# Optimization experiments

Measured on AMD Instinct MI355X. Metric: run time of the kernel, lower is better.

## Reference

```python
import jax, jax.numpy as jnp
import numpy as np

B, Q, S, D, H = 8, 100, 4096, 256, 8
HD = D // H
EPS = 1e-5


def layer_norm(x, g, b):
    mu = jnp.mean(x, axis=-1, keepdims=True)
    var = jnp.mean(jnp.square(x - mu), axis=-1, keepdims=True)
    return (x - mu) * jax.lax.rsqrt(var + EPS) * g + b


def mha(q_in, k_in, v_in, w_in, b_in, w_out, b_out, bias=None):
    # torch nn.MultiheadAttention math (batch_first, dropout=0)
    wq, wk, wv = jnp.split(w_in, 3, axis=0)
    bq, bk, bv = jnp.split(b_in, 3, axis=0)
    Bq, Lq, _ = q_in.shape
    Lk = k_in.shape[1]
    q = (q_in @ wq.T + bq).reshape(Bq, Lq, H, HD)
    k = (k_in @ wk.T + bk).reshape(Bq, Lk, H, HD)
    v = (v_in @ wv.T + bv).reshape(Bq, Lk, H, HD)
    scores = jnp.einsum('bqhd,bkhd->bhqk', q, k) / jnp.sqrt(jnp.asarray(HD, q.dtype))
    if bias is not None:
        scores = scores + bias  # [B,1,Q,S] broadcast over heads (same per head)
    attn = jax.nn.softmax(scores, axis=-1)
    out = jnp.einsum('bhqk,bkhd->bqhd', attn, v).reshape(Bq, Lq, D)
    return out @ w_out.T + b_out


def setup_inputs() -> dict:
    key = jax.random.key(0)
    ks = jax.random.split(key, 12)
    s = 0.02
    return {
        'queries': jax.random.normal(ks[0], (B, Q, D), jnp.float32),
        'pixel_feat': jax.random.normal(ks[1], (B, S, D), jnp.float32),
        'prev_mask': jax.random.normal(ks[2], (B, Q, S), jnp.float32),
        'cross_in_w': jax.random.normal(ks[3], (3 * D, D), jnp.float32) * s,
        'cross_in_b': jnp.zeros((3 * D,), jnp.float32),
        'cross_out_w': jax.random.normal(ks[4], (D, D), jnp.float32) * s,
        'cross_out_b': jnp.zeros((D,), jnp.float32),
        'self_in_w': jax.random.normal(ks[5], (3 * D, D), jnp.float32) * s,
        'self_in_b': jnp.zeros((3 * D,), jnp.float32),
        'self_out_w': jax.random.normal(ks[6], (D, D), jnp.float32) * s,
        'self_out_b': jnp.zeros((D,), jnp.float32),
        'ln_cross_g': jnp.ones((D,), jnp.float32),
        'ln_cross_b': jnp.zeros((D,), jnp.float32),
        'ln_self_g': jnp.ones((D,), jnp.float32),
        'ln_self_b': jnp.zeros((D,), jnp.float32),
        'ln_ffn_g': jnp.ones((D,), jnp.float32),
        'ln_ffn_b': jnp.zeros((D,), jnp.float32),
        'ffn_w1': jax.random.normal(ks[7], (4 * D, D), jnp.float32) * s,
        'ffn_b1': jnp.zeros((4 * D,), jnp.float32),
        'ffn_w2': jax.random.normal(ks[8], (D, 4 * D), jnp.float32) * s,
        'ffn_b2': jnp.zeros((D,), jnp.float32),
    }


def reference(queries, pixel_feat, prev_mask,
              cross_in_w, cross_in_b, cross_out_w, cross_out_b,
              self_in_w, self_in_b, self_out_w, self_out_b,
              ln_cross_g, ln_cross_b, ln_self_g, ln_self_b, ln_ffn_g, ln_ffn_b,
              ffn_w1, ffn_b1, ffn_w2, ffn_b2):
    # masked cross-attn bias (no-grad region in torch; boolean ops have no grad)
    region = jax.nn.sigmoid(prev_mask) > 0.5                    # [B,Q,S]
    any_pos = jnp.any(region, axis=-1, keepdims=True)
    region = jnp.where(any_pos, region, jnp.ones_like(region))
    bias = (~region).astype(queries.dtype) * -10000.0
    bias = bias[:, None, :, :]                                  # [B,1,Q,S]

    q_out = mha(layer_norm(queries, ln_cross_g, ln_cross_b), pixel_feat, pixel_feat,
                cross_in_w, cross_in_b, cross_out_w, cross_out_b, bias)
    queries = queries + q_out

    q_norm = layer_norm(queries, ln_self_g, ln_self_b)
    q_out = mha(q_norm, q_norm, q_norm, self_in_w, self_in_b, self_out_w, self_out_b)
    queries = queries + q_out

    h = layer_norm(queries, ln_ffn_g, ln_ffn_b)
    h = jax.nn.gelu(h @ ffn_w1.T + ffn_b1, approximate=False) @ ffn_w2.T + ffn_b2
    return queries + h
```

## Files before the change

### kernel.cpp

```cpp
#include <hip/hip_runtime.h>
#include <hip/hip_bf16.h>
#include <math.h>

#define BQ 100
#define SB 8
#define SS 4096
#define DD 256
#define HH 8
#define HDD 32
#define NSPLIT 4
#define SCHUNK (SS / NSPLIT)
#define MROWS 800

typedef __attribute__((ext_vector_type(8))) short bf16x8;
typedef __attribute__((ext_vector_type(4))) float f32x4;

__device__ inline unsigned short f2bf(float f) {
    union { float f; unsigned u; } v; v.f = f;
    unsigned r = v.u + 0x7fff + ((v.u >> 16) & 1);
    return (unsigned short)(r >> 16);
}

__device__ inline unsigned pkbf(float x, float y) {
    union { __hip_bfloat162 h; unsigned u; } c;
    c.h = __float22bfloat162_rn(make_float2(x, y));
    return c.u;
}

__device__ inline bf16x8 load_bf8(const float* p) {
    float4 a = *(const float4*)p;
    float4 b = *(const float4*)(p + 4);
    union { unsigned u[4]; bf16x8 v; } r;
    r.u[0] = pkbf(a.x, a.y); r.u[1] = pkbf(a.z, a.w);
    r.u[2] = pkbf(b.x, b.y); r.u[3] = pkbf(b.z, b.w);
    return r.v;
}

typedef __attribute__((address_space(1))) const void gas_void;
typedef __attribute__((address_space(3))) void las_void;
__device__ inline void gl_lds16(const unsigned short* g, unsigned short* l) {
    __builtin_amdgcn_global_load_lds((gas_void*)g, (las_void*)l, 16, 0, 0);
}

#define TM 128
#define TN 128

#define WOFF_CW   0
#define WOFF_SIW  196608
#define WOFF_COW  393216
#define WOFF_SOW  458752
#define WOFF_F1   524288
#define WOFF_F2   786432
#define WTOT      1048576

__global__ __launch_bounds__(256) void wprep(
        const float* __restrict__ cw, const float* __restrict__ siw,
        const float* __restrict__ cow, const float* __restrict__ sow,
        const float* __restrict__ f1, const float* __restrict__ f2,
        const float* __restrict__ pix,
        unsigned short* __restrict__ o, unsigned short* __restrict__ abf) {
    int b = blockIdx.x;
    int t = threadIdx.x;
    if (b >= 512) {
        size_t off = (size_t)(b - 512) * 2048 + (size_t)t * 8;
        const float* p = pix + off;
        float4 a = *(const float4*)p;
        float4 c = *(const float4*)(p + 4);
        uint4 pk;
        pk.x = pkbf(a.x, a.y); pk.y = pkbf(a.z, a.w);
        pk.z = pkbf(c.x, c.y); pk.w = pkbf(c.z, c.w);
        *(uint4*)(abf + off) = pk;
        return;
    }
    const float* src; size_t so, doff;
    if (b < 96)       { src = cw;  so = (size_t)b * 2048;         doff = WOFF_CW; }
    else if (b < 192) { src = siw; so = (size_t)(b - 96) * 2048;  doff = WOFF_SIW; }
    else if (b < 224) { src = cow; so = (size_t)(b - 192) * 2048; doff = WOFF_COW; }
    else if (b < 256) { src = sow; so = (size_t)(b - 224) * 2048; doff = WOFF_SOW; }
    else if (b < 384) { src = f1;  so = (size_t)(b - 256) * 2048; doff = WOFF_F1; }
    else              { src = f2;  so = (size_t)(b - 384) * 2048; doff = WOFF_F2; }
    const float* p = src + so + (size_t)t * 8;
    float4 a = *(const float4*)p;
    float4 c = *(const float4*)(p + 4);
    uint4 pk;
    pk.x = pkbf(a.x, a.y); pk.y = pkbf(a.z, a.w);
    pk.z = pkbf(c.x, c.y); pk.w = pkbf(c.z, c.w);
    *(uint4*)(o + doff + so + (size_t)t * 8) = pk;
}

__global__ __launch_bounds__(256, 3) void stage1(
        const float* __restrict__ queries,
        const float* __restrict__ ln_g, const float* __restrict__ ln_b,
        const unsigned short* __restrict__ wbf,
        const float* __restrict__ cb,
        float* __restrict__ q_cross,
        const unsigned short* __restrict__ Abf,
        unsigned short* __restrict__ Kb, unsigned short* __restrict__ Vb,
        const float* __restrict__ mask, unsigned* __restrict__ Mbits) {
    __shared__ __align__(16) char smem[32768];
    const int bid = blockIdx.x;
    const int t = threadIdx.x;

    if (bid < 1024) {
        unsigned short* Sbuf = (unsigned short*)smem;
        const unsigned short* Wb = wbf + (size_t)DD * DD;
        const float* bias = cb + DD;
        int xcd = bid & 7, idx = bid >> 3;
        int mtile = xcd + 8 * (idx >> 2);
        int ntl = idx & 3;
        int m0 = mtile * TM, n0 = ntl * TN;
        int wave = t >> 6, lane = t & 63;
        int wm = (wave & 1) * 64, wn = (wave >> 1) * 64;
        int fr = lane & 15, quad = lane >> 4;
        f32x4 acc[4][4] = {};

        const int c0 = t, c1 = 256 + t;
        const int r0 = c0 >> 2, r1 = c1 >> 2;
        const int cc0 = (c0 & 3) ^ ((r0 >> 1) & 3);
        const int cc1 = (c1 & 3) ^ ((r1 >> 1) & 3);

        gl_lds16(Abf + (size_t)(m0 + r0) * DD + cc0 * 8, Sbuf + c0 * 8);
        gl_lds16(Abf + (size_t)(m0 + r1) * DD + cc1 * 8, Sbuf + c1 * 8);
        gl_lds16(Wb + (size_t)(n0 + r0) * DD + cc0 * 8, Sbuf + 4096 + c0 * 8);
        gl_lds16(Wb + (size_t)(n0 + r1) * DD + cc1 * 8, Sbuf + 4096 + c1 * 8);
        __syncthreads();

#pragma unroll
        for (int ks = 0; ks < 8; ks++) {
            unsigned short* Ab = Sbuf + (ks & 1) * 8192;
            unsigned short* Bb = Ab + 4096;
            if (ks < 7) {
                unsigned short* An = Sbuf + ((ks + 1) & 1) * 8192;
                unsigned short* Bn = An + 4096;
                int k0 = (ks + 1) * 32;
                gl_lds16(Abf + (size_t)(m0 + r0) * DD + k0 + cc0 * 8, An + c0 * 8);
                gl_lds16(Abf + (size_t)(m0 + r1) * DD + k0 + cc1 * 8, An + c1 * 8);
                gl_lds16(Wb + (size_t)(n0 + r0) * DD + k0 + cc0 * 8, Bn + c0 * 8);
                gl_lds16(Wb + (size_t)(n0 + r1) * DD + k0 + cc1 * 8, Bn + c1 * 8);
            }
            bf16x8 af[4], bv[4];
#pragma unroll
            for (int mi = 0; mi < 4; mi++) {
                int row = wm + mi * 16 + fr;
                int j = quad ^ ((row >> 1) & 3);
                af[mi] = *(const bf16x8*)(Ab + row * 32 + j * 8);
            }
#pragma unroll
            for (int ni = 0; ni < 4; ni++) {
                int row = wn + ni * 16 + fr;
                int j = quad ^ ((row >> 1) & 3);
                bv[ni] = *(const bf16x8*)(Bb + row * 32 + j * 8);
            }
#pragma unroll
            for (int mi = 0; mi < 4; mi++) {
                acc[mi][0] = __builtin_amdgcn_mfma_f32_16x16x32_bf16(af[mi], bv[0], acc[mi][0], 0, 0, 0);
                acc[mi][1] = __builtin_amdgcn_mfma_f32_16x16x32_bf16(af[mi], bv[1], acc[mi][1], 0, 0, 0);
                acc[mi][2] = __builtin_amdgcn_mfma_f32_16x16x32_bf16(af[mi], bv[2], acc[mi][2], 0, 0, 0);
                acc[mi][3] = __builtin_amdgcn_mfma_f32_16x16x32_bf16(af[mi], bv[3], acc[mi][3], 0, 0, 0);
            }
            __syncthreads();
        }
#pragma unroll
        for (int ni = 0; ni < 4; ni++) {
            int n = n0 + wn + ni * 16 + fr;
            float bv = bias[n];
            unsigned short* dst = (n < 256) ? Kb : Vb;
            int hh = (n >> 5) & 7, d = n & 31;
#pragma unroll
            for (int mi = 0; mi < 4; mi++) {
#pragma unroll
                for (int r = 0; r < 4; r++) {
                    int m = m0 + wm + mi * 16 + quad * 4 + r;
                    int bb = m >> 12, s = m & (SS - 1);
                    dst[((((size_t)bb * HH + hh) * SS + s) << 5) + d] =
                        f2bf(acc[mi][ni][r] + bv);
                }
            }
        }
    } else if (bid < 1824) {
        int row = bid - 1024;
        unsigned* words = (unsigned*)smem;
        unsigned* orred = (unsigned*)(smem + 512);
        int w = t >> 6, lane = t & 63;
        const float* mp = mask + (size_t)row * SS + lane;
        float mv[16];
#pragma unroll
        for (int i = 0; i < 16; i++) mv[i] = mp[(w * 16 + i) * 64];
        unsigned lor = 0;
#pragma unroll
        for (int i = 0; i < 16; i++) {
            unsigned long long bal = __ballot(mv[i] > 0.f);
            if (lane == 0) {
                words[(w * 16 + i) * 2] = (unsigned)bal;
                words[(w * 16 + i) * 2 + 1] = (unsigned)(bal >> 32);
            }
            lor |= (unsigned)(bal | (bal >> 32));
        }
        if (lane == 0) orred[w] = lor;
        __syncthreads();
        unsigned anyv = orred[0] | orred[1] | orred[2] | orred[3];
        if (t < 128) Mbits[(size_t)row * 128 + t] = anyv ? words[t] : 0xFFFFFFFFu;
    } else {
        typedef unsigned short (*arow_t)[264];
        arow_t Aq = (arow_t)smem;
        float* mu_s = (float*)(smem + 16896);
        float* rs_s = mu_s + 32;
        float (*prt)[8][2] = (float(*)[8][2])(rs_s + 32);
        int idx = bid - 1824;
        int nq = idx & 1, my = idx >> 1;
        int m0 = my * 32;
        int row = t & 31, cs = t >> 5;
        const float* xp = queries + (size_t)(m0 + row) * DD + cs * 32;
        float s = 0.f, ss = 0.f;
#pragma unroll
        for (int c = 0; c < 32; c += 4) {
            float4 v = *(const float4*)(xp + c);
            s += v.x + v.y + v.z + v.w;
            ss += v.x * v.x + v.y * v.y + v.z * v.z + v.w * v.w;
        }
        prt[row][cs][0] = s; prt[row][cs][1] = ss;
        __syncthreads();
        if (t < 32) {
            float sum = 0.f, sq = 0.f;
#pragma unroll
            for (int k = 0; k < 8; k++) { sum += prt[t][k][0]; sq += prt[t][k][1]; }
            float mu = sum * (1.0f / DD);
            float var = sq * (1.0f / DD) - mu * mu;
            mu_s[t] = mu;
            rs_s[t] = rsqrtf(var + 1e-5f);
        }
        __syncthreads();
        {
            float mu = mu_s[row], r = rs_s[row];
            int col0 = cs * 32;
#pragma unroll
            for (int c = 0; c < 32; c += 8) {
                int col = col0 + c;
                float4 v0 = *(const float4*)(xp + c);
                float4 v1 = *(const float4*)(xp + c + 4);
                float4 g0 = *(const float4*)(ln_g + col);
                float4 g1 = *(const float4*)(ln_g + col + 4);
                float4 b0 = *(const float4*)(ln_b + col);
                float4 b1 = *(const float4*)(ln_b + col + 4);
                uint4 pk;
                pk.x = pkbf((v0.x - mu) * r * g0.x + b0.x, (v0.y - mu) * r * g0.y + b0.y);
                pk.y = pkbf((v0.z - mu) * r * g0.z + b0.z, (v0.w - mu) * r * g0.w + b0.w);
                pk.z = pkbf((v1.x - mu) * r * g1.x + b1.x, (v1.y - mu) * r * g1.y + b1.y);
                pk.w = pkbf((v1.z - mu) * r * g1.z + b1.z, (v1.w - mu) * r * g1.w + b1.w);
                *(uint4*)&Aq[row][col] = pk;
            }
        }
        __syncthreads();
        int w = t >> 6, lane = t & 63;
        int fr = lane & 15, quad = lane >> 4;
        int n0 = nq * 128 + w * 32;
        f32x4 acc[2][2] = {};
        const unsigned short* Wq0 = wbf + (size_t)(n0 + fr) * DD + quad * 8;
        const unsigned short* Wq1 = Wq0 + (size_t)16 * DD;
#pragma unroll
        for (int k0 = 0; k0 < DD; k0 += 32) {
            bf16x8 a0 = *(const bf16x8*)&Aq[fr][k0 + quad * 8];
            bf16x8 a1 = *(const bf16x8*)&Aq[16 + fr][k0 + quad * 8];
            bf16x8 w0 = *(const bf16x8*)(Wq0 + k0);
            bf16x8 w1 = *(const bf16x8*)(Wq1 + k0);
            acc[0][0] = __builtin_amdgcn_mfma_f32_16x16x32_bf16(a0, w0, acc[0][0], 0, 0, 0);
            acc[0][1] = __builtin_amdgcn_mfma_f32_16x16x32_bf16(a0, w1, acc[0][1], 0, 0, 0);
            acc[1][0] = __builtin_amdgcn_mfma_f32_16x16x32_bf16(a1, w0, acc[1][0], 0, 0, 0);
            acc[1][1] = __builtin_amdgcn_mfma_f32_16x16x32_bf16(a1, w1, acc[1][1], 0, 0, 0);
        }
#pragma unroll
        for (int ni = 0; ni < 2; ni++) {
            int n = n0 + ni * 16 + fr;
            float bv = cb[n];
#pragma unroll
            for (int mi = 0; mi < 2; mi++) {
#pragma unroll
                for (int r = 0; r < 4; r++) {
                    int m = m0 + mi * 16 + quad * 4 + r;
                    q_cross[(size_t)m * DD + n] = acc[mi][ni][r] + bv;
                }
            }
        }
    }
}

template<int MODE>
__global__ __launch_bounds__(64, 4) void ln_gemm(
        const float* __restrict__ X, const float* __restrict__ gam,
        const float* __restrict__ bet,
        const unsigned short* __restrict__ W, const float* __restrict__ bias,
        const float* __restrict__ res,
        float* __restrict__ C, int N) {
    __shared__ unsigned short As[32][264];
    __shared__ float mu_s[32], rs_s[32];
    __shared__ float prt[32][2][2];
    const int t = threadIdx.x;
    const int fr = t & 15, quad = t >> 4;
    const int m0 = blockIdx.y * 32, n0 = blockIdx.x * 32;
    const int row = t & 31, half = t >> 5;

    const float* xp = X + (size_t)(m0 + row) * DD + half * 128;
    float s = 0.f, ss = 0.f;
#pragma unroll
    for (int c = 0; c < 128; c += 4) {
        float4 v = *(const float4*)(xp + c);
        s += v.x + v.y + v.z + v.w;
        ss += v.x * v.x + v.y * v.y + v.z * v.z + v.w * v.w;
    }
    prt[row][half][0] = s;
    prt[row][half][1] = ss;
    __syncthreads();
    if (t < 32) {
        float sum = prt[t][0][0] + prt[t][1][0];
        float sq  = prt[t][0][1] + prt[t][1][1];
        float mu = sum * (1.0f / DD);
        float var = sq * (1.0f / DD) - mu * mu;
        mu_s[t] = mu;
        rs_s[t] = rsqrtf(var + 1e-5f);
    }
    __syncthreads();
    {
        float mu = mu_s[row], r = rs_s[row];
#pragma unroll
        for (int c = 0; c < 128; c += 8) {
            int col = half * 128 + c;
            float4 v0 = *(const float4*)(xp + c);
            float4 v1 = *(const float4*)(xp + c + 4);
            float4 g0 = *(const float4*)(gam + col);
            float4 g1 = *(const float4*)(gam + col + 4);
            float4 b0 = *(const float4*)(bet + col);
            float4 b1 = *(const float4*)(bet + col + 4);
            uint4 pk;
            pk.x = pkbf((v0.x - mu) * r * g0.x + b0.x, (v0.y - mu) * r * g0.y + b0.y);
            pk.y = pkbf((v0.z - mu) * r * g0.z + b0.z, (v0.w - mu) * r * g0.w + b0.w);
            pk.z = pkbf((v1.x - mu) * r * g1.x + b1.x, (v1.y - mu) * r * g1.y + b1.y);
            pk.w = pkbf((v1.z - mu) * r * g1.z + b1.z, (v1.w - mu) * r * g1.w + b1.w);
            *(uint4*)&As[row][col] = pk;
        }
    }
    __syncthreads();

    f32x4 acc[2][2] = {};
    const unsigned short* Wp0 = W + (size_t)(n0 + fr) * DD + quad * 8;
    const unsigned short* Wp1 = Wp0 + (size_t)16 * DD;
#pragma unroll
    for (int k0 = 0; k0 < DD; k0 += 32) {
        bf16x8 a0 = *(const bf16x8*)&As[fr][k0 + quad * 8];
        bf16x8 a1 = *(const bf16x8*)&As[16 + fr][k0 + quad * 8];
        bf16x8 w0 = *(const bf16x8*)(Wp0 + k0);
        bf16x8 w1 = *(const bf16x8*)(Wp1 + k0);
        acc[0][0] = __builtin_amdgcn_mfma_f32_16x16x32_bf16(a0, w0, acc[0][0], 0, 0, 0);
        acc[0][1] = __builtin_amdgcn_mfma_f32_16x16x32_bf16(a0, w1, acc[0][1], 0, 0, 0);
        acc[1][0] = __builtin_amdgcn_mfma_f32_16x16x32_bf16(a1, w0, acc[1][0], 0, 0, 0);
        acc[1][1] = __builtin_amdgcn_mfma_f32_16x16x32_bf16(a1, w1, acc[1][1], 0, 0, 0);
    }

#pragma unroll
    for (int ni = 0; ni < 2; ni++) {
        int n = n0 + ni * 16 + fr;
        float bv = bias[n];
#pragma unroll
        for (int mi = 0; mi < 2; mi++) {
#pragma unroll
            for (int r = 0; r < 4; r++) {
                int m = m0 + mi * 16 + quad * 4 + r;
                float v = acc[mi][ni][r] + bv;
                if (MODE == 1) {
                    v = 0.5f * v * (1.0f + erff(v * 0.70710678118654752f));
                } else if (MODE == 2) {
                    v += res[(size_t)m * N + n];
                }
                C[(size_t)m * N + n] = v;
            }
        }
    }
}

__global__ __launch_bounds__(64, 4) void comb_gemm(
        const float* __restrict__ Opart, const float* __restrict__ mpart,
        const float* __restrict__ lpart,
        const unsigned short* __restrict__ W, const float* __restrict__ bias,
        const float* __restrict__ res,
        float* __restrict__ C) {
    __shared__ unsigned short As[32][264];
    const int t = threadIdx.x;
    const int fr = t & 15, quad = t >> 4;
    const int m0 = blockIdx.y * 32, n0 = blockIdx.x * 32;
    const int row = t & 31, half = t >> 5;

    {
        int m = m0 + row;
        int b = m / BQ, q = m % BQ;
#pragma unroll
        for (int h = half * 4; h < half * 4 + 4; h++) {
            float mv[NSPLIT], wsp[NSPLIT];
            float mstar = -1e30f;
#pragma unroll
            for (int sp = 0; sp < NSPLIT; sp++) {
                mv[sp] = mpart[((size_t)(b * NSPLIT + sp) * HH + h) * BQ + q];
                mstar = fmaxf(mstar, mv[sp]);
            }
            float lstar = 0.f;
#pragma unroll
            for (int sp = 0; sp < NSPLIT; sp++) {
                wsp[sp] = __expf(mv[sp] - mstar);
                lstar += lpart[((size_t)(b * NSPLIT + sp) * HH + h) * BQ + q] * wsp[sp];
            }
            float inv = 1.0f / lstar;
#pragma unroll
            for (int d = 0; d < HDD; d += 8) {
                float o[8] = {};
#pragma unroll
                for (int sp = 0; sp < NSPLIT; sp++) {
                    const float* op = Opart +
                        ((size_t)(b * NSPLIT + sp) * BQ + q) * DD + h * HDD + d;
                    float4 a = *(const float4*)op;
                    float4 b4 = *(const float4*)(op + 4);
                    o[0] += a.x * wsp[sp];  o[1] += a.y * wsp[sp];
                    o[2] += a.z * wsp[sp];  o[3] += a.w * wsp[sp];
                    o[4] += b4.x * wsp[sp]; o[5] += b4.y * wsp[sp];
                    o[6] += b4.z * wsp[sp]; o[7] += b4.w * wsp[sp];
                }
                uint4 pk;
                pk.x = pkbf(o[0] * inv, o[1] * inv);
                pk.y = pkbf(o[2] * inv, o[3] * inv);
                pk.z = pkbf(o[4] * inv, o[5] * inv);
                pk.w = pkbf(o[6] * inv, o[7] * inv);
                *(uint4*)&As[row][h * HDD + d] = pk;
            }
        }
    }
    __syncthreads();

    f32x4 acc[2][2] = {};
    const unsigned short* Wp0 = W + (size_t)(n0 + fr) * DD + quad * 8;
    const unsigned short* Wp1 = Wp0 + (size_t)16 * DD;
#pragma unroll
    for (int k0 = 0; k0 < DD; k0 += 32) {
        bf16x8 a0 = *(const bf16x8*)&As[fr][k0 + quad * 8];
        bf16x8 a1 = *(const bf16x8*)&As[16 + fr][k0 + quad * 8];
        bf16x8 w0 = *(const bf16x8*)(Wp0 + k0);
        bf16x8 w1 = *(const bf16x8*)(Wp1 + k0);
        acc[0][0] = __builtin_amdgcn_mfma_f32_16x16x32_bf16(a0, w0, acc[0][0], 0, 0, 0);
        acc[0][1] = __builtin_amdgcn_mfma_f32_16x16x32_bf16(a0, w1, acc[0][1], 0, 0, 0);
        acc[1][0] = __builtin_amdgcn_mfma_f32_16x16x32_bf16(a1, w0, acc[1][0], 0, 0, 0);
        acc[1][1] = __builtin_amdgcn_mfma_f32_16x16x32_bf16(a1, w1, acc[1][1], 0, 0, 0);
    }

#pragma unroll
    for (int ni = 0; ni < 2; ni++) {
        int n = n0 + ni * 16 + fr;
        float bv = bias[n];
#pragma unroll
        for (int mi = 0; mi < 2; mi++) {
#pragma unroll
            for (int r = 0; r < 4; r++) {
                int m = m0 + mi * 16 + quad * 4 + r;
                float v = acc[mi][ni][r] + bv + res[(size_t)m * DD + n];
                C[(size_t)m * DD + n] = v;
            }
        }
    }
}

template<int KK, int SPLITK, int MODE>
__global__ __launch_bounds__(64, 4) void gemm_skinny2(
        const float* __restrict__ A, const unsigned short* __restrict__ W,
        const float* __restrict__ bias, const float* __restrict__ res,
        float* __restrict__ C, float* __restrict__ Cp, int N) {
    const int lane = threadIdx.x;
    const int fr = lane & 15, quad = lane >> 4;
    const int m0 = blockIdx.y * 32;
    const int n0 = blockIdx.x * 32;
    const int sk = blockIdx.z;
    const int KCH = KK / SPLITK;

    f32x4 acc[2][2] = {};
    const float* Ap0 = A + (size_t)(m0 + fr) * KK + sk * KCH + quad * 8;
    const float* Ap1 = Ap0 + (size_t)16 * KK;
    const unsigned short* Wp0 = W + (size_t)(n0 + fr) * KK + sk * KCH + quad * 8;
    const unsigned short* Wp1 = Wp0 + (size_t)16 * KK;

#pragma unroll
    for (int k0 = 0; k0 < KCH; k0 += 32) {
        bf16x8 a0 = load_bf8(Ap0 + k0);
        bf16x8 a1 = load_bf8(Ap1 + k0);
        bf16x8 w0 = *(const bf16x8*)(Wp0 + k0);
        bf16x8 w1 = *(const bf16x8*)(Wp1 + k0);
        acc[0][0] = __builtin_amdgcn_mfma_f32_16x16x32_bf16(a0, w0, acc[0][0], 0, 0, 0);
        acc[0][1] = __builtin_amdgcn_mfma_f32_16x16x32_bf16(a0, w1, acc[0][1], 0, 0, 0);
        acc[1][0] = __builtin_amdgcn_mfma_f32_16x16x32_bf16(a1, w0, acc[1][0], 0, 0, 0);
        acc[1][1] = __builtin_amdgcn_mfma_f32_16x16x32_bf16(a1, w1, acc[1][1], 0, 0, 0);
    }

    if (SPLITK == 1) {
#pragma unroll
        for (int ni = 0; ni < 2; ni++) {
            int n = n0 + ni * 16 + fr;
            float bv = bias[n];
#pragma unroll
            for (int mi = 0; mi < 2; mi++) {
#pragma unroll
                for (int r = 0; r < 4; r++) {
                    int m = m0 + mi * 16 + quad * 4 + r;
                    float v = acc[mi][ni][r] + bv;
                    if (MODE == 1) {
                        v = 0.5f * v * (1.0f + erff(v * 0.70710678118654752f));
                    } else if (MODE == 2) {
                        v += res[(size_t)m * N + n];
                    }
                    C[(size_t)m * N + n] = v;
                }
            }
        }
    } else {
        float* dst = Cp + (size_t)sk * MROWS * N;
#pragma unroll
        for (int ni = 0; ni < 2; ni++) {
            int n = n0 + ni * 16 + fr;
#pragma unroll
            for (int mi = 0; mi < 2; mi++) {
#pragma unroll
                for (int r = 0; r < 4; r++) {
                    int m = m0 + mi * 16 + quad * 4 + r;
                    dst[(size_t)m * N + n] = acc[mi][ni][r];
                }
            }
        }
    }
}

template<int SPLITK, int MODE>
__global__ void gemm_combine(const float* __restrict__ Cp,
                             const float* __restrict__ bias,
                             const float* __restrict__ res,
                             float* __restrict__ C, int N) {
    int m = blockIdx.x;
    for (int n = threadIdx.x; n < N; n += 256) {
        float v = bias[n];
#pragma unroll
        for (int sk = 0; sk < SPLITK; sk++)
            v += Cp[((size_t)sk * MROWS + m) * N + n];
        if (MODE == 1) {
            v = 0.5f * v * (1.0f + erff(v * 0.70710678118654752f));
        } else if (MODE == 2) {
            v += res[(size_t)m * N + n];
        }
        C[(size_t)m * N + n] = v;
    }
}

#define QT 64
#define ST 128

__global__ __launch_bounds__(256) void cross_attn_mfma(
        const float* __restrict__ Qm,
        const unsigned short* __restrict__ Kb,
        const unsigned short* __restrict__ Vb,
        const unsigned* __restrict__ Mbits,
        float* __restrict__ Opart,
        float* __restrict__ mpart,
        float* __restrict__ lpart) {
    __shared__ unsigned short Qs[QT][40];
    __shared__ unsigned short Ks[ST][40];
    __shared__ unsigned short Vt[HDD][136];
    __shared__ unsigned short Ps[QT][136];
    __shared__ unsigned Mq[QT][4];
    __shared__ float red[QT][17];
    __shared__ float m_s[QT], alpha_s[QT], l_s[QT];

    const int qb = blockIdx.x, h = blockIdx.y;
    const int b = blockIdx.z / NSPLIT, sp = blockIdx.z % NSPLIT;
    const int t = threadIdx.x;
    const int w = t >> 6, lane = t & 63;
    const int fr = lane & 15, quad = lane >> 4;
    const int q0 = qb * QT;
    const int qlim = min(BQ - q0, QT);

    {
        int q = t >> 2, c0 = (t & 3) * 8;
        float4 v0 = make_float4(0.f, 0.f, 0.f, 0.f), v1 = v0;
        if (q < qlim) {
            const float* qp = Qm + (size_t)(b * BQ + q0 + q) * DD + h * HDD + c0;
            v0 = *(const float4*)qp;
            v1 = *(const float4*)(qp + 4);
        }
        const float sc = 0.17677669529663687f;
        uint4 pq;
        pq.x = pkbf(v0.x * sc, v0.y * sc);
        pq.y = pkbf(v0.z * sc, v0.w * sc);
        pq.z = pkbf(v1.x * sc, v1.y * sc);
        pq.w = pkbf(v1.z * sc, v1.w * sc);
        *(uint4*)&Qs[q][c0] = pq;
        if (t < QT) { m_s[t] = -1e30f; l_s[t] = 0.f; }
    }

    f32x4 oacc[2] = {};
    const unsigned short* Kbase = Kb + (((size_t)(b * HH + h)) * SS << 5);
    const unsigned short* Vbase = Vb + (((size_t)(b * HH + h)) * SS << 5);

    for (int s0 = sp * SCHUNK; s0 < (sp + 1) * SCHUNK; s0 += ST) {
        __syncthreads();
        {
            int r = t >> 1, half = t & 1;
            const unsigned short* kp = Kbase + ((size_t)(s0 + r) << 5) + half * 16;
            *(uint4*)&Ks[r][half * 16] = *(const uint4*)kp;
            *(uint4*)&Ks[r][half * 16 + 8] = *(const uint4*)(kp + 8);
            const unsigned short* vp = Vbase + ((size_t)(s0 + r) << 5) + half * 16;
            union { uint4 u; unsigned short s[8]; } v0, v1;
            v0.u = *(const uint4*)vp;
            v1.u = *(const uint4*)(vp + 8);
#pragma unroll
            for (int j = 0; j < 8; j++) Vt[half * 16 + j][r] = v0.s[j];
#pragma unroll
            for (int j = 0; j < 8; j++) Vt[half * 16 + 8 + j][r] = v1.s[j];
        }
        {
            int q = t >> 2, wd = t & 3;
            unsigned mword = 0xFFFFFFFFu;
            if (q < qlim)
                mword = Mbits[(size_t)(b * BQ + q0 + q) * 128 + (s0 >> 5) + wd];
            Mq[q][wd] = mword;
        }
        __syncthreads();

        bf16x8 af[2];
#pragma unroll
        for (int mt = 0; mt < 2; mt++)
            af[mt] = *(const bf16x8*)&Ks[w * 32 + mt * 16 + fr][quad * 8];
        f32x4 st[2][4];
#pragma unroll
        for (int nt = 0; nt < 4; nt++) {
            bf16x8 bq = *(const bf16x8*)&Qs[nt * 16 + fr][quad * 8];
#pragma unroll
            for (int mt = 0; mt < 2; mt++) {
                f32x4 z = {0.f, 0.f, 0.f, 0.f};
                st[mt][nt] = __builtin_amdgcn_mfma_f32_16x16x32_bf16(af[mt], bq, z, 0, 0, 0);
            }
        }

        float pmax[4] = {-1e30f, -1e30f, -1e30f, -1e30f};
#pragma unroll
        for (int nt = 0; nt < 4; nt++) {
            unsigned mword = Mq[nt * 16 + fr][w];
#pragma unroll
            for (int mt = 0; mt < 2; mt++)
#pragma unroll
                for (int r = 0; r < 4; r++) {
                    int bitpos = mt * 16 + quad * 4 + r;
                    float v = st[mt][nt][r];
                    if (!((mword >> bitpos) & 1u)) v -= 10000.f;
                    st[mt][nt][r] = v;
                    pmax[nt] = fmaxf(pmax[nt], v);
                }
        }
#pragma unroll
        for (int nt = 0; nt < 4; nt++)
            red[nt * 16 + fr][w * 4 + quad] = pmax[nt];
        __syncthreads();

        if (t < QT) {
            float mt_ = -1e30f;
#pragma unroll
            for (int k = 0; k < 16; k++) mt_ = fmaxf(mt_, red[t][k]);
            float mo = m_s[t], mn = fmaxf(mo, mt_);
            m_s[t] = mn;
            alpha_s[t] = __expf(mo - mn);
        }
        __syncthreads();

        float psum[4] = {0.f, 0.f, 0.f, 0.f};
#pragma unroll
        for (int nt = 0; nt < 4; nt++) {
            float mrow = m_s[nt * 16 + fr];
#pragma unroll
            for (int mt = 0; mt < 2; mt++) {
                float p0 = __expf(st[mt][nt][0] - mrow);
                float p1 = __expf(st[mt][nt][1] - mrow);
                float p2 = __expf(st[mt][nt][2] - mrow);
                float p3 = __expf(st[mt][nt][3] - mrow);
                psum[nt] += p0 + p1 + p2 + p3;
                uint2 pk;
                pk.x = pkbf(p0, p1);
                pk.y = pkbf(p2, p3);
                *(uint2*)&Ps[nt * 16 + fr][w * 32 + mt * 16 + quad * 4] = pk;
            }
        }
#pragma unroll
        for (int nt = 0; nt < 4; nt++)
            red[nt * 16 + fr][w * 4 + quad] = psum[nt];
        __syncthreads();

        if (t < QT) {
            float s = 0.f;
#pragma unroll
            for (int k = 0; k < 16; k++) s += red[t][k];
            l_s[t] = l_s[t] * alpha_s[t] + s;
        }

#pragma unroll
        for (int r = 0; r < 4; r++) {
            float a = alpha_s[w * 16 + quad * 4 + r];
            oacc[0][r] *= a; oacc[1][r] *= a;
        }
#pragma unroll
        for (int k0 = 0; k0 < ST; k0 += 32) {
            bf16x8 ap = *(const bf16x8*)&Ps[w * 16 + fr][k0 + quad * 8];
            bf16x8 bv0 = *(const bf16x8*)&Vt[fr][k0 + quad * 8];
            bf16x8 bv1 = *(const bf16x8*)&Vt[16 + fr][k0 + quad * 8];
            oacc[0] = __builtin_amdgcn_mfma_f32_16x16x32_bf16(ap, bv0, oacc[0], 0, 0, 0);
            oacc[1] = __builtin_amdgcn_mfma_f32_16x16x32_bf16(ap, bv1, oacc[1], 0, 0, 0);
        }
    }
    __syncthreads();

    int part = b * NSPLIT + sp;
    if (t < qlim) {
        mpart[((size_t)part * HH + h) * BQ + q0 + t] = m_s[t];
        lpart[((size_t)part * HH + h) * BQ + q0 + t] = l_s[t];
    }
#pragma unroll
    for (int nd = 0; nd < 2; nd++) {
#pragma unroll
        for (int r = 0; r < 4; r++) {
            int q = w * 16 + quad * 4 + r;
            if (q < qlim)
                Opart[((size_t)part * BQ + q0 + q) * DD + h * HDD + nd * 16 + fr] = oacc[nd][r];
        }
    }
}

__global__ __launch_bounds__(256) void self_attn_mfma(
        const float* __restrict__ qkv, float* __restrict__ Out) {
    __shared__ unsigned short Qs[128][40];
    __shared__ unsigned short Vt[HDD][136];
    __shared__ unsigned short Ps[112][136];
    __shared__ float red[112][17];
    __shared__ float m_s[112], l_s[112];

    const int h = blockIdx.x, b = blockIdx.y;
    const int t = threadIdx.x;
    const int w = t >> 6, lane = t & 63;
    const int fr = lane & 15, quad = lane >> 4;
    const float sc = 0.17677669529663687f;

    {
        int r = t >> 1, half = t & 1;
        float4 a0 = make_float4(0.f, 0.f, 0.f, 0.f), a1 = a0, a2 = a0, a3 = a0;
        float4 c0 = a0, c1 = a0, c2 = a0, c3 = a0;
        if (r < BQ) {
            const float* qp = qkv + (size_t)(b * BQ + r) * 768 + h * HDD + half * 16;
            a0 = *(const float4*)qp;       a1 = *(const float4*)(qp + 4);
            a2 = *(const float4*)(qp + 8); a3 = *(const float4*)(qp + 12);
            const float* vp = qp + 512;
            c0 = *(const float4*)vp;       c1 = *(const float4*)(vp + 4);
            c2 = *(const float4*)(vp + 8); c3 = *(const float4*)(vp + 12);
        }
        uint4 p0, p1;
        p0.x = pkbf(a0.x * sc, a0.y * sc); p0.y = pkbf(a0.z * sc, a0.w * sc);
        p0.z = pkbf(a1.x * sc, a1.y * sc); p0.w = pkbf(a1.z * sc, a1.w * sc);
        p1.x = pkbf(a2.x * sc, a2.y * sc); p1.y = pkbf(a2.z * sc, a2.w * sc);
        p1.z = pkbf(a3.x * sc, a3.y * sc); p1.w = pkbf(a3.z * sc, a3.w * sc);
        *(uint4*)&Qs[r][half * 16] = p0;
        *(uint4*)&Qs[r][half * 16 + 8] = p1;
        float vv[16] = {c0.x, c0.y, c0.z, c0.w, c1.x, c1.y, c1.z, c1.w,
                        c2.x, c2.y, c2.z, c2.w, c3.x, c3.y, c3.z, c3.w};
#pragma unroll
        for (int j = 0; j < 16; j++) Vt[half * 16 + j][r] = f2bf(vv[j]);
    }
    __syncthreads();

    bf16x8 af[2];
#pragma unroll
    for (int mt = 0; mt < 2; mt++) {
        int s = w * 32 + mt * 16 + fr;
        bf16x8 kz = {0, 0, 0, 0, 0, 0, 0, 0};
        af[mt] = kz;
        if (s < BQ)
            af[mt] = load_bf8(qkv + (size_t)(b * BQ + s) * 768 + 256 + h * HDD + quad * 8);
    }
    f32x4 st[2][7];
#pragma unroll
    for (int nt = 0; nt < 7; nt++) {
        bf16x8 bq = *(const bf16x8*)&Qs[nt * 16 + fr][quad * 8];
#pragma unroll
        for (int mt = 0; mt < 2; mt++) {
            f32x4 z = {0.f, 0.f, 0.f, 0.f};
            st[mt][nt] = __builtin_amdgcn_mfma_f32_16x16x32_bf16(af[mt], bq, z, 0, 0, 0);
        }
    }

    float pmax[7];
#pragma unroll
    for (int nt = 0; nt < 7; nt++) {
        pmax[nt] = -1e30f;
#pragma unroll
        for (int mt = 0; mt < 2; mt++)
#pragma unroll
            for (int r = 0; r < 4; r++) {
                int s = w * 32 + mt * 16 + quad * 4 + r;
                float v = st[mt][nt][r];
                if (s >= BQ) v = -1e30f;
                st[mt][nt][r] = v;
                pmax[nt] = fmaxf(pmax[nt], v);
            }
        red[nt * 16 + fr][w * 4 + quad] = pmax[nt];
    }
    __syncthreads();
    if (t < 112) {
        float m = -1e30f;
#pragma unroll
        for (int k = 0; k < 16; k++) m = fmaxf(m, red[t][k]);
        m_s[t] = m;
    }
    __syncthreads();

    float psum[7];
#pragma unroll
    for (int nt = 0; nt < 7; nt++) {
        float mrow = m_s[nt * 16 + fr];
        psum[nt] = 0.f;
#pragma unroll
        for (int mt = 0; mt < 2; mt++) {
            float p0 = __expf(st[mt][nt][0] - mrow);
            float p1 = __expf(st[mt][nt][1] - mrow);
            float p2 = __expf(st[mt][nt][2] - mrow);
            float p3 = __expf(st[mt][nt][3] - mrow);
            psum[nt] += p0 + p1 + p2 + p3;
            uint2 pk;
            pk.x = pkbf(p0, p1);
            pk.y = pkbf(p2, p3);
            *(uint2*)&Ps[nt * 16 + fr][w * 32 + mt * 16 + quad * 4] = pk;
        }
        red[nt * 16 + fr][w * 4 + quad] = psum[nt];
    }
    __syncthreads();
    if (t < 112) {
        float s = 0.f;
#pragma unroll
        for (int k = 0; k < 16; k++) s += red[t][k];
        l_s[t] = s;
    }
    __syncthreads();

    f32x4 oacc[2][2] = {};
#pragma unroll
    for (int ti = 0; ti < 2; ti++) {
        int qt = w + ti * 4;
        if (qt < 7) {
#pragma unroll
            for (int k0 = 0; k0 < 128; k0 += 32) {
                bf16x8 ap = *(const bf16x8*)&Ps[qt * 16 + fr][k0 + quad * 8];
                bf16x8 bv0 = *(const bf16x8*)&Vt[fr][k0 + quad * 8];
                bf16x8 bv1 = *(const bf16x8*)&Vt[16 + fr][k0 + quad * 8];
                oacc[ti][0] = __builtin_amdgcn_mfma_f32_16x16x32_bf16(ap, bv0, oacc[ti][0], 0, 0, 0);
                oacc[ti][1] = __builtin_amdgcn_mfma_f32_16x16x32_bf16(ap, bv1, oacc[ti][1], 0, 0, 0);
            }
        }
    }
#pragma unroll
    for (int ti = 0; ti < 2; ti++) {
        int qt = w + ti * 4;
        if (qt < 7) {
#pragma unroll
            for (int nd = 0; nd < 2; nd++) {
#pragma unroll
                for (int r = 0; r < 4; r++) {
                    int q = qt * 16 + quad * 4 + r;
                    if (q < BQ) {
                        float inv = 1.0f / l_s[q];
                        Out[(size_t)(b * BQ + q) * DD + h * HDD + nd * 16 + fr] =
                            oacc[ti][nd][r] * inv;
                    }
                }
            }
        }
    }
}

extern "C" void kernel_launch(void* const* d_in, const int* in_sizes, int n_in,
                              void* d_out, int out_size, void* d_ws, size_t ws_size,
                              hipStream_t stream) {
    const float* queries    = (const float*)d_in[0];
    const float* pixel_feat = (const float*)d_in[1];
    const float* prev_mask  = (const float*)d_in[2];
    const float* cross_in_w  = (const float*)d_in[3];
    const float* cross_in_b  = (const float*)d_in[4];
    const float* cross_out_w = (const float*)d_in[5];
    const float* cross_out_b = (const float*)d_in[6];
    const float* self_in_w   = (const float*)d_in[7];
    const float* self_in_b   = (const float*)d_in[8];
    const float* self_out_w  = (const float*)d_in[9];
    const float* self_out_b  = (const float*)d_in[10];
    const float* ln_cross_g  = (const float*)d_in[11];
    const float* ln_cross_b  = (const float*)d_in[12];
    const float* ln_self_g   = (const float*)d_in[13];
    const float* ln_self_b   = (const float*)d_in[14];
    const float* ln_ffn_g    = (const float*)d_in[15];
    const float* ln_ffn_b    = (const float*)d_in[16];
    const float* ffn_w1 = (const float*)d_in[17];
    const float* ffn_b1 = (const float*)d_in[18];
    const float* ffn_w2 = (const float*)d_in[19];
    const float* ffn_b2 = (const float*)d_in[20];
    float* out = (float*)d_out;

    const int NQ = SB * BQ;
    const int NK = SB * SS;

    float* ws = (float*)d_ws;
    unsigned* Mbits = (unsigned*)ws;   ws += (size_t)NQ * 128;
    float* q_cross  = ws;              ws += (size_t)NQ * DD;
    unsigned short* Kbk = (unsigned short*)ws;
    ws += (size_t)NK * DD / 2;
    unsigned short* Vbk = (unsigned short*)ws;
    ws += (size_t)NK * DD / 2;
    float* queries1 = ws;              ws += (size_t)NQ * DD;
    float* qkv      = ws;              ws += (size_t)NQ * 3 * DD;
    float* attn2    = ws;              ws += (size_t)NQ * DD;
    float* queries2 = ws;              ws += (size_t)NQ * DD;
    float* ffn_h    = ws;              ws += (size_t)NQ * 4 * DD;
    float* Csplit   = ws;              ws += (size_t)4 * MROWS * DD;
    float* Opart    = ws;              ws += (size_t)SB * NSPLIT * BQ * DD;
    float* mpart    = ws;              ws += (size_t)SB * NSPLIT * HH * BQ;
    float* lpart    = ws;              ws += (size_t)SB * NSPLIT * HH * BQ;
    unsigned short* wbf = (unsigned short*)ws;
    ws += WTOT / 2;
    unsigned short* Abf = (unsigned short*)ws;

    const float scale = 0.17677669529663687f;
    (void)scale;

    wprep<<<4608, 256, 0, stream>>>(
        cross_in_w, self_in_w, cross_out_w, self_out_w, ffn_w1, ffn_w2,
        pixel_feat, wbf, Abf);

    stage1<<<1874, 256, 0, stream>>>(
        queries, ln_cross_g, ln_cross_b, wbf, cross_in_b, q_cross,
        Abf, Kbk, Vbk, prev_mask, Mbits);

    cross_attn_mfma<<<dim3(2, HH, SB * NSPLIT), 256, 0, stream>>>(
        q_cross, Kbk, Vbk, Mbits, Opart, mpart, lpart);
    comb_gemm<<<dim3(8, 25), 64, 0, stream>>>(
        Opart, mpart, lpart, wbf + WOFF_COW, cross_out_b, queries, queries1);

    ln_gemm<0><<<dim3(24, 25), 64, 0, stream>>>(
        queries1, ln_self_g, ln_self_b, wbf + WOFF_SIW, self_in_b, nullptr,
        qkv, 3 * DD);
    self_attn_mfma<<<dim3(HH, SB), 256, 0, stream>>>(qkv, attn2);
    gemm_skinny2<256, 1, 2><<<dim3(8, 25), 64, 0, stream>>>(
        attn2, wbf + WOFF_SOW, self_out_b, queries1, queries2, nullptr, DD);

    ln_gemm<1><<<dim3(32, 25), 64, 0, stream>>>(
        queries2, ln_ffn_g, ln_ffn_b, wbf + WOFF_F1, ffn_b1, nullptr,
        ffn_h, 4 * DD);
    gemm_skinny2<1024, 4, 2><<<dim3(8, 25, 4), 64, 0, stream>>>(
        ffn_h, wbf + WOFF_F2, ffn_b2, nullptr, nullptr, Csplit, DD);
    gemm_combine<4, 2><<<MROWS, 256, 0, stream>>>(
        Csplit, ffn_b2, queries2, out, DD);
}
```

Baseline: 230.7 us.

## Double cross-attn split count and reduce softmax stats via wave shuffles

The number of sequence splits for the cross-attention kernel rises from 4 to 8, doubling the grid to raise parallelism, at the cost of more partial outputs for the combine kernel to merge. Inside the kernel, row max and row sum are now reduced with wave shuffles before a single small shared-memory write. Every thread then computes the new max and alpha redundantly, which removes one __syncthreads barrier per S-tile and the serial 16-way shared reductions. The alpha_s write now happens without a barrier before it is read in the output rescale, which relies on the next barrier ordering it.

```diff
diff --git a/kernel.cpp b/kernel.cpp
--- a/kernel.cpp
+++ b/kernel.cpp
@@ -8,7 +8,7 @@
 #define DD 256
 #define HH 8
 #define HDD 32
-#define NSPLIT 4
+#define NSPLIT 8
 #define SCHUNK (SS / NSPLIT)
 #define MROWS 800
 
@@ -566,7 +566,8 @@
     __shared__ unsigned short Vt[HDD][136];
     __shared__ unsigned short Ps[QT][136];
     __shared__ unsigned Mq[QT][4];
-    __shared__ float red[QT][17];
+    __shared__ float4 redm[QT];
+    __shared__ float4 reds[QT];
     __shared__ float m_s[QT], alpha_s[QT], l_s[QT];
 
     const int qb = blockIdx.x, h = blockIdx.y;
@@ -639,10 +640,15 @@
             }
         }
 
-        float pmax[4] = {-1e30f, -1e30f, -1e30f, -1e30f};
+        float mo[4];
+#pragma unroll
+        for (int nt = 0; nt < 4; nt++) mo[nt] = m_s[nt * 16 + fr];
+
+        float pmax[4];
 #pragma unroll
         for (int nt = 0; nt < 4; nt++) {
             unsigned mword = Mq[nt * 16 + fr][w];
+            pmax[nt] = -1e30f;
 #pragma unroll
             for (int mt = 0; mt < 2; mt++)
 #pragma unroll
@@ -655,30 +661,43 @@
                 }
         }
 #pragma unroll
-        for (int nt = 0; nt < 4; nt++)
-            red[nt * 16 + fr][w * 4 + quad] = pmax[nt];
+        for (int nt = 0; nt < 4; nt++) {
+            pmax[nt] = fmaxf(pmax[nt], __shfl_xor(pmax[nt], 16));
+            pmax[nt] = fmaxf(pmax[nt], __shfl_xor(pmax[nt], 32));
+        }
+        if (quad == 0) {
+#pragma unroll
+            for (int nt = 0; nt < 4; nt++)
+                ((float*)&redm[nt * 16 + fr])[w] = pmax[nt];
+        }
         __syncthreads();
 
-        if (t < QT) {
-            float mt_ = -1e30f;
-#pragma unroll
-            for (int k = 0; k < 16; k++) mt_ = fmaxf(mt_, red[t][k]);
-            float mo = m_s[t], mn = fmaxf(mo, mt_);
-            m_s[t] = mn;
-            alpha_s[t] = __expf(mo - mn);
-        }
-        __syncthreads();
-
-        float psum[4] = {0.f, 0.f, 0.f, 0.f};
+        float mn[4], al[4];
 #pragma unroll
         for (int nt = 0; nt < 4; nt++) {
-            float mrow = m_s[nt * 16 + fr];
+            float4 rr = redm[nt * 16 + fr];
+            float mt4 = fmaxf(fmaxf(rr.x, rr.y), fmaxf(rr.z, rr.w));
+            mn[nt] = fmaxf(mo[nt], mt4);
+            al[nt] = __expf(mo[nt] - mn[nt]);
+        }
+        if (w == 0 && quad == 0) {
+#pragma unroll
+            for (int nt = 0; nt < 4; nt++) {
+                m_s[nt * 16 + fr] = mn[nt];
+                alpha_s[nt * 16 + fr] = al[nt];
+            }
+        }
+
+        float psum[4];
+#pragma unroll
+        for (int nt = 0; nt < 4; nt++) {
+            psum[nt] = 0.f;
 #pragma unroll
             for (int mt = 0; mt < 2; mt++) {
-                float p0 = __expf(st[mt][nt][0] - mrow);
-                float p1 = __expf(st[mt][nt][1] - mrow);
-                float p2 = __expf(st[mt][nt][2] - mrow);
-                float p3 = __expf(st[mt][nt][3] - mrow);
+                float p0 = __expf(st[mt][nt][0] - mn[nt]);
+                float p1 = __expf(st[mt][nt][1] - mn[nt]);
+                float p2 = __expf(st[mt][nt][2] - mn[nt]);
+                float p3 = __expf(st[mt][nt][3] - mn[nt]);
                 psum[nt] += p0 + p1 + p2 + p3;
                 uint2 pk;
                 pk.x = pkbf(p0, p1);
@@ -687,15 +706,24 @@
             }
         }
 #pragma unroll
-        for (int nt = 0; nt < 4; nt++)
-            red[nt * 16 + fr][w * 4 + quad] = psum[nt];
+        for (int nt = 0; nt < 4; nt++) {
+            psum[nt] += __shfl_xor(psum[nt], 16);
+            psum[nt] += __shfl_xor(psum[nt], 32);
+        }
+        if (quad == 0) {
+#pragma unroll
+            for (int nt = 0; nt < 4; nt++)
+                ((float*)&reds[nt * 16 + fr])[w] = psum[nt];
+        }
         __syncthreads();
 
-        if (t < QT) {
-            float s = 0.f;
-#pragma unroll
-            for (int k = 0; k < 16; k++) s += red[t][k];
-            l_s[t] = l_s[t] * alpha_s[t] + s;
+        if (w == 0 && quad == 0) {
+#pragma unroll
+            for (int nt = 0; nt < 4; nt++) {
+                int q = nt * 16 + fr;
+                float4 ssum = reds[q];
+                l_s[q] = l_s[q] * al[nt] + (ssum.x + ssum.y + ssum.z + ssum.w);
+            }
         }
 
 #pragma unroll
@@ -927,9 +955,6 @@
     ws += WTOT / 2;
     unsigned short* Abf = (unsigned short*)ws;
 
-    const float scale = 0.17677669529663687f;
-    (void)scale;
-
     wprep<<<4608, 256, 0, stream>>>(
         cross_in_w, self_in_w, cross_out_w, self_out_w, ffn_w1, ffn_w2,
         pixel_feat, wbf, Abf);
```

After: 236.2 us. 1.02x slower.
